# Performance work log

Hardware: AMD Instinct MI355X
Metric: run time of the kernel (lower is better)

The kernel has to match this reference:

```python
import jax, jax.numpy as jnp
import numpy as np

B, I, O, G, D = 2048, 128, 128, 8, 2  # batch, input_dim, output_dim, num_grids, num_dim (complex algebra)
RHO = 1.0
EPS = 1e-5  # BatchNorm1d default eps
GRID_MIN, GRID_MAX = -2.0, 2.0


def _make_cayley():
    # Complex-number geometric algebra: metric=[-1], basis {1, e1}, e1*e1 = -1.
    # (a*b)_z = sum_{x,y} a_x b_y C[x,y,z]
    C = np.zeros((2, 2, 2), dtype=np.float32)
    C[0, 0, 0] = 1.0
    C[0, 1, 1] = 1.0
    C[1, 0, 1] = 1.0
    C[1, 1, 0] = -1.0
    return jnp.asarray(C)


def _make_grid():
    # create_grid2d_full: real varies along axis 0, imag along axis 1 -> (G, G, 2)
    g = jnp.linspace(GRID_MIN, GRID_MAX, G)
    gr, gi = jnp.meshgrid(g, g, indexing='ij')
    return jnp.stack((gr, gi), axis=-1)


def setup_inputs() -> dict:
    key = jax.random.key(0)
    k1, k2 = jax.random.split(key)
    x = jax.random.normal(k1, (B, I, D), dtype=jnp.float32)
    weights = jax.random.normal(k2, (I, O, G, G, D), dtype=jnp.float32)
    silu_weight = jnp.ones((I, O, D), dtype=jnp.float32)
    silu_bias = jnp.zeros((I, O, D), dtype=jnp.float32)
    gamma = jnp.ones((D,), dtype=jnp.float32)   # BatchNorm weight (componentwise)
    beta = jnp.zeros((D,), dtype=jnp.float32)   # BatchNorm bias
    return {
        'x': x,
        'weights': weights,
        'silu_weight': silu_weight,
        'silu_bias': silu_bias,
        'gamma': gamma,
        'beta': beta,
        'grid': _make_grid(),
        'cayley': _make_cayley(),
    }


def reference(x, weights, silu_weight, silu_bias, gamma, beta, grid, cayley):
    # RBF expansion: exp(-||x - grid_point||^2 / rho), complex-algebra norm^2 = a^2 + b^2
    diff = x[:, :, None, None, :] - grid[None, None, :, :, :]        # (B, I, G, G, D)
    rbf = jnp.exp(-jnp.sum(diff * diff, axis=-1) / RHO)              # (B, I, G, G)
    # grid-weight contraction
    res = jnp.einsum('biuv,iouvx->biox', rbf, weights)               # (B, I, O, D)
    # componentwise SiLU branch with Cayley-table (complex) multiplication
    s = jax.nn.silu(x)                                               # (B, I, D)
    sv = jnp.einsum('iox,biy,xyz->bioz', silu_weight, s, cayley)     # (B, I, O, D)
    sv = sv + silu_bias
    out = jnp.sum(res + sv, axis=1)                                  # (B, O, D) -- 'biox->box'
    # componentwise BatchNorm (training mode): stats over (B, O) per component
    mean = jnp.mean(out, axis=(0, 1))
    var = jnp.var(out, axis=(0, 1))
    out = gamma * (out - mean) * jax.lax.rsqrt(var + EPS) + beta
    return out
```

## Files before the change

kernel.cpp:

```cpp
#include <hip/hip_runtime.h>
#include <stdint.h>

typedef unsigned short u16;
typedef __attribute__((ext_vector_type(8))) short bf16x8;
typedef __attribute__((ext_vector_type(4))) float f32x4;

#define B_      2048
#define I_      128
#define O_      128
#define K_MAIN  8192
#define K_TOT   8448
#define N_      256
#define BO      262144
#define NSLICE  16
#define KSTEPS  132

#define W_OFF      0u
#define W_BYTES    (256u*8448u*2u)
#define OUTPS_OFF  (W_OFF + W_BYTES)
#define OUTPS_BYTES (16u*524288u*4u)
#define OUTRED_OFF (OUTPS_OFF + OUTPS_BYTES)
#define OUTRED_BYTES (524288u*4u)
#define BSUM_OFF   (OUTRED_OFF + OUTRED_BYTES)
#define STATS_OFF  (BSUM_OFF + 1024u)

__device__ __forceinline__ float bf2f(u16 u) {
    union { unsigned int i; float f; } c; c.i = ((unsigned int)u) << 16; return c.f;
}
__device__ __forceinline__ u16 f2bf(float f) {
    unsigned int u = __float_as_uint(f);
    return (u16)((u + 0x7fffu + ((u >> 16) & 1u)) >> 16);
}
__device__ __forceinline__ unsigned int pkbf(float lo, float hi) {
    unsigned int ul = __float_as_uint(lo), uh = __float_as_uint(hi);
    ul += 0x7fffu + ((ul >> 16) & 1u);
    uh += 0x7fffu + ((uh >> 16) & 1u);
    return __builtin_amdgcn_perm(uh, ul, 0x07060302);
}
__device__ __forceinline__ float loadF(const void* p, long idx, bool isbf) {
    return isbf ? bf2f(((const u16*)p)[idx]) : ((const float*)p)[idx];
}

#define GLD16(gsrc, ldst) __builtin_amdgcn_global_load_lds( \
    (const __attribute__((address_space(1))) void*)(gsrc),  \
    (__attribute__((address_space(3))) void*)(ldst), 16, 0, 0)

__global__ __launch_bounds__(256) void pack_w(const void* wgt, const void* sw,
                                              const void* sb, u16* W, float* bsum,
                                              float* stats, const u16* flag) {
    bool isbf = (flag[0] == 0x3F80u);
    if (blockIdx.x < 1024) {
        int gid = blockIdx.x * 256 + threadIdx.x;
        int t8 = gid & 15;
        int io = gid >> 4;
        int i = io >> 7, o = io & 127;
        int base = t8 * 8;
        int u = base >> 4, v0 = (base & 15) >> 1;
        long off = ((long)i * 128 + o) * 128 + base;
        float f[8];
        if (isbf) {
            uint4 raw = *(const uint4*)((const u16*)wgt + off);
            const u16* h = (const u16*)&raw;
#pragma unroll
            for (int j = 0; j < 8; ++j) f[j] = bf2f(h[j]);
        } else {
            float4 a = *(const float4*)((const float*)wgt + off);
            float4 bq = *(const float4*)((const float*)wgt + off + 4);
            f[0]=a.x; f[1]=a.y; f[2]=a.z; f[3]=a.w;
            f[4]=bq.x; f[5]=bq.y; f[6]=bq.z; f[7]=bq.w;
        }
        u16 re[4], im[4];
#pragma unroll
        for (int j = 0; j < 4; ++j) { re[j] = f2bf(f[2*j]); im[j] = f2bf(f[2*j+1]); }
        int k = i * 64 + u * 8 + v0;
        *(uint2*)&W[(size_t)(2*o)     * K_TOT + k] = *(const uint2*)re;
        *(uint2*)&W[(size_t)(2*o + 1) * K_TOT + k] = *(const uint2*)im;
    } else if (blockIdx.x < 1280) {
        int e = (blockIdx.x - 1024) * 256 + threadIdx.x;
        int n = e >> 8, j = e & 255;
        int o = n >> 1, xc = n & 1;
        int i = j >> 1, c = j & 1;
        float swr = loadF(sw, (long)(i * 128 + o) * 2, isbf);
        float swi = loadF(sw, (long)(i * 128 + o) * 2 + 1, isbf);
        float v = (xc == 0) ? (c == 0 ? swr : -swi) : (c == 0 ? swi : swr);
        W[(size_t)n * K_TOT + K_MAIN + j] = f2bf(v);
    } else {
        int n = threadIdx.x;
        float s = 0.0f;
#pragma unroll 8
        for (int i = 0; i < 128; ++i) s += loadF(sb, (long)i * 256 + n, isbf);
        bsum[n] = s;
        if (threadIdx.x < 4) stats[threadIdx.x] = 0.0f;
    }
}

#define BM 64
#define BN 256
#define BK 64

__global__ __launch_bounds__(256, 2) void gemm_fused(const void* __restrict__ x,
                                                     const void* __restrict__ grd,
                                                     const u16* __restrict__ W,
                                                     float* __restrict__ out_ps,
                                                     const u16* flag) {
    bool isbf = (flag[0] == 0x3F80u);
    __shared__ u16 As[BM * BK];
    __shared__ u16 Bs[BN * BK];
    int tid = threadIdx.x, lane = tid & 63, w = tid >> 6;
    int wm = w >> 1, wn = w & 1;
    int m0 = blockIdx.y * BM;
    int s = blockIdx.z;
    int quad = lane >> 4, l16 = lane & 15;
    int arow = tid >> 2, q4 = tid & 3;
    int asw = arow & 7;
    int kbeg = (KSTEPS * s) / NSLICE, kend = (KSTEPS * (s + 1)) / NSLICE;

    float g[8];
#pragma unroll
    for (int j = 0; j < 8; ++j) g[j] = loadF(grd, (long)j * 16, isbf);

    f32x4 zero = {0.f, 0.f, 0.f, 0.f};
    f32x4 acc[2][8];
#pragma unroll
    for (int mt = 0; mt < 2; ++mt)
#pragma unroll
        for (int nt = 0; nt < 8; ++nt) acc[mt][nt] = zero;

    for (int kt = kbeg; kt < kend; ++kt) {
        int k0 = kt * 64;
#pragma unroll
        for (int jj = 0; jj < 8; ++jj) {
            int p = (w * 8 + jj) * 64 + lane;
            int r = p >> 3, cph = p & 7;
            int c = cph ^ (r & 7);
            GLD16(W + (size_t)r * K_TOT + k0 + c * 8,
                  Bs + (size_t)p * 8);
        }
        unsigned int op[8];
        if (kt < 128) {
            long xb = ((long)(m0 + arow) * 128 + kt) * 2;
            float vr = loadF(x, xb, isbf);
            float vi = loadF(x, xb + 1, isbf);
            float ei[8];
#pragma unroll
            for (int v = 0; v < 8; ++v) { float d = vi - g[v]; ei[v] = __expf(-d * d); }
#pragma unroll
            for (int uu = 0; uu < 2; ++uu) {
                float d = vr - g[2 * q4 + uu];
                float er = __expf(-d * d);
#pragma unroll
                for (int v = 0; v < 8; v += 2)
                    op[uu * 4 + (v >> 1)] = pkbf(er * ei[v], er * ei[v + 1]);
            }
        } else {
            int t = kt - 128;
            long base = (long)(m0 + arow) * 256 + 64 * t + 16 * q4;
#pragma unroll
            for (int e = 0; e < 16; e += 2) {
                float v0 = loadF(x, base + e, isbf);
                float v1 = loadF(x, base + e + 1, isbf);
                float s0 = v0 / (1.0f + __expf(-v0));
                float s1 = v1 / (1.0f + __expf(-v1));
                op[e >> 1] = pkbf(s0, s1);
            }
        }
        {
            u16* rowbase = As + arow * 64;
            *(uint4*)(rowbase + (((2 * q4)     ^ asw) << 3)) = ((const uint4*)op)[0];
            *(uint4*)(rowbase + (((2 * q4 + 1) ^ asw) << 3)) = ((const uint4*)op)[1];
        }
        __syncthreads();
#pragma unroll
        for (int ks = 0; ks < 2; ++ks) {
            bf16x8 fa[2], fb[8];
#pragma unroll
            for (int mt = 0; mt < 2; ++mt) {
                int r = wm * 32 + mt * 16 + l16;
                fa[mt] = *(const bf16x8*)&As[r * 64 + (((ks * 4 + quad) ^ (r & 7)) << 3)];
            }
#pragma unroll
            for (int nt = 0; nt < 8; ++nt) {
                int r = wn * 128 + nt * 16 + l16;
                fb[nt] = *(const bf16x8*)&Bs[r * 64 + (((ks * 4 + quad) ^ (r & 7)) << 3)];
            }
#pragma unroll
            for (int mt = 0; mt < 2; ++mt)
#pragma unroll
                for (int nt = 0; nt < 8; ++nt)
                    acc[mt][nt] = __builtin_amdgcn_mfma_f32_16x16x32_bf16(
                        fa[mt], fb[nt], acc[mt][nt], 0, 0, 0);
        }
        __syncthreads();
    }
    float* outp = out_ps + (size_t)s * 524288;
    int mbase = m0 + wm * 32 + quad * 4;
    int nbase = wn * 128 + l16;
#pragma unroll
    for (int mt = 0; mt < 2; ++mt)
#pragma unroll
        for (int nt = 0; nt < 8; ++nt) {
            int n = nbase + nt * 16;
#pragma unroll
            for (int r = 0; r < 4; ++r) {
                int m = mbase + mt * 16 + r;
                outp[(size_t)m * N_ + n] = acc[mt][nt][r];
            }
        }
}

__global__ void stats_red(const float* __restrict__ out_ps, const float* __restrict__ bsum,
                          float* __restrict__ out_red, float* stats) {
    int gid = blockIdx.x * 256 + threadIdx.x;
    int o = gid & 127;
    float vr = 0.f, vi = 0.f;
#pragma unroll
    for (int s = 0; s < NSLICE; ++s) {
        float2 p = *(const float2*)(out_ps + (size_t)s * 524288 + (size_t)gid * 2);
        vr += p.x; vi += p.y;
    }
    vr += bsum[o * 2]; vi += bsum[o * 2 + 1];
    float2 ov; ov.x = vr; ov.y = vi;
    *(float2*)(out_red + (size_t)gid * 2) = ov;
    float sr = vr, si = vi, qr = vr * vr, qi = vi * vi;
    for (int off = 32; off > 0; off >>= 1) {
        sr += __shfl_down(sr, off);
        si += __shfl_down(si, off);
        qr += __shfl_down(qr, off);
        qi += __shfl_down(qi, off);
    }
    __shared__ float red[4][4];
    int lane = threadIdx.x & 63, w = threadIdx.x >> 6;
    if (lane == 0) { red[w][0] = sr; red[w][1] = si; red[w][2] = qr; red[w][3] = qi; }
    __syncthreads();
    if (threadIdx.x < 4) {
        float t = red[0][threadIdx.x] + red[1][threadIdx.x] +
                  red[2][threadIdx.x] + red[3][threadIdx.x];
        atomicAdd(&stats[threadIdx.x], t);
    }
}

__global__ void norm_k(const float* __restrict__ out_red, const float* __restrict__ stats,
                       const void* gamma, const void* beta, void* out, const u16* flag) {
    bool isbf = (flag[0] == 0x3F80u);
    int gid = blockIdx.x * 256 + threadIdx.x;
    const float inv = 1.0f / (float)BO;
    float mr = stats[0] * inv, mi = stats[1] * inv;
    float varr = stats[2] * inv - mr * mr;
    float vari = stats[3] * inv - mi * mi;
    float gr = loadF(gamma, 0, isbf), gi = loadF(gamma, 1, isbf);
    float br = loadF(beta, 0, isbf),  bi = loadF(beta, 1, isbf);
    float scr = gr * rsqrtf(varr + 1e-5f);
    float sci = gi * rsqrtf(vari + 1e-5f);
    float2 v = *(const float2*)(out_red + (size_t)gid * 2);
    float rr = (v.x - mr) * scr + br;
    float ri = (v.y - mi) * sci + bi;
    if (isbf) {
        unsigned int packed = pkbf(rr, ri);
        *(unsigned int*)((u16*)out + (size_t)gid * 2) = packed;
    } else {
        ((float*)out)[(size_t)gid * 2]     = rr;
        ((float*)out)[(size_t)gid * 2 + 1] = ri;
    }
}

extern "C" void kernel_launch(void* const* d_in, const int* in_sizes, int n_in,
                              void* d_out, int out_size, void* d_ws, size_t ws_size,
                              hipStream_t stream) {
    const void* x     = d_in[0];
    const void* wgt   = d_in[1];
    const void* sw    = d_in[2];
    const void* sb    = d_in[3];
    const void* gamma = d_in[4];
    const void* beta  = d_in[5];
    const void* grd   = d_in[6];
    const u16* flag = (const u16*)gamma;

    uint8_t* ws = (uint8_t*)d_ws;
    u16*   W       = (u16*)(ws + W_OFF);
    float* out_ps  = (float*)(ws + OUTPS_OFF);
    float* out_red = (float*)(ws + OUTRED_OFF);
    float* bsum    = (float*)(ws + BSUM_OFF);
    float* stats   = (float*)(ws + STATS_OFF);

    pack_w<<<1281, 256, 0, stream>>>(wgt, sw, sb, W, bsum, stats, flag);
    gemm_fused<<<dim3(1, B_ / BM, NSLICE), 256, 0, stream>>>(x, grd, W, out_ps, flag);
    stats_red<<<1024, 256, 0, stream>>>(out_ps, bsum, out_red, stats);
    norm_k<<<1024, 256, 0, stream>>>(out_red, stats, gamma, beta, d_out, flag);
}
```

Measured before the change: 132.3 us.

## Reduce split-K partial sums with global atomics instead of a partial buffer

The GEMM slices no longer write per-slice partial outputs to a 16x workspace that a separate pass then sums. Each slice now atomically adds its results straight into a single zero-initialised output buffer, which the weight-pack kernel clears. The stats kernel only reads the reduced values, and the bias sum is applied in both stats and normalisation. This removes the large partial write and reread, but adds 16-way float atomic contention per element and makes the summation order nondeterministic.

```diff
diff --git a/kernel.cpp b/kernel.cpp
--- a/kernel.cpp
+++ b/kernel.cpp
@@ -17,9 +17,7 @@
 
 #define W_OFF      0u
 #define W_BYTES    (256u*8448u*2u)
-#define OUTPS_OFF  (W_OFF + W_BYTES)
-#define OUTPS_BYTES (16u*524288u*4u)
-#define OUTRED_OFF (OUTPS_OFF + OUTPS_BYTES)
+#define OUTRED_OFF (W_OFF + W_BYTES)
 #define OUTRED_BYTES (524288u*4u)
 #define BSUM_OFF   (OUTRED_OFF + OUTRED_BYTES)
 #define STATS_OFF  (BSUM_OFF + 1024u)
@@ -47,7 +45,8 @@
 
 __global__ __launch_bounds__(256) void pack_w(const void* wgt, const void* sw,
                                               const void* sb, u16* W, float* bsum,
-                                              float* stats, const u16* flag) {
+                                              float* stats, float* out_red,
+                                              const u16* flag) {
     bool isbf = (flag[0] == 0x3F80u);
     if (blockIdx.x < 1024) {
         int gid = blockIdx.x * 256 + threadIdx.x;
@@ -84,13 +83,17 @@
         float swi = loadF(sw, (long)(i * 128 + o) * 2 + 1, isbf);
         float v = (xc == 0) ? (c == 0 ? swr : -swi) : (c == 0 ? swi : swr);
         W[(size_t)n * K_TOT + K_MAIN + j] = f2bf(v);
-    } else {
+    } else if (blockIdx.x == 1280) {
         int n = threadIdx.x;
         float s = 0.0f;
 #pragma unroll 8
         for (int i = 0; i < 128; ++i) s += loadF(sb, (long)i * 256 + n, isbf);
         bsum[n] = s;
         if (threadIdx.x < 4) stats[threadIdx.x] = 0.0f;
+    } else {
+        int g2 = (blockIdx.x - 1281) * 256 + threadIdx.x;
+        float2 z; z.x = 0.f; z.y = 0.f;
+        *(float2*)(out_red + (size_t)g2 * 2) = z;
     }
 }
 
@@ -101,7 +104,7 @@
 __global__ __launch_bounds__(256, 2) void gemm_fused(const void* __restrict__ x,
                                                      const void* __restrict__ grd,
                                                      const u16* __restrict__ W,
-                                                     float* __restrict__ out_ps,
+                                                     float* __restrict__ out_red,
                                                      const u16* flag) {
     bool isbf = (flag[0] == 0x3F80u);
     __shared__ u16 As[BM * BK];
@@ -192,7 +195,6 @@
         }
         __syncthreads();
     }
-    float* outp = out_ps + (size_t)s * 524288;
     int mbase = m0 + wm * 32 + quad * 4;
     int nbase = wn * 128 + l16;
 #pragma unroll
@@ -203,24 +205,18 @@
 #pragma unroll
             for (int r = 0; r < 4; ++r) {
                 int m = mbase + mt * 16 + r;
-                outp[(size_t)m * N_ + n] = acc[mt][nt][r];
-            }
-        }
-}
-
-__global__ void stats_red(const float* __restrict__ out_ps, const float* __restrict__ bsum,
-                          float* __restrict__ out_red, float* stats) {
+                atomicAdd(&out_red[(size_t)m * N_ + n], acc[mt][nt][r]);
+            }
+        }
+}
+
+__global__ void stats_k(const float* __restrict__ out_red, const float* __restrict__ bsum,
+                        float* stats) {
     int gid = blockIdx.x * 256 + threadIdx.x;
     int o = gid & 127;
-    float vr = 0.f, vi = 0.f;
-#pragma unroll
-    for (int s = 0; s < NSLICE; ++s) {
-        float2 p = *(const float2*)(out_ps + (size_t)s * 524288 + (size_t)gid * 2);
-        vr += p.x; vi += p.y;
-    }
-    vr += bsum[o * 2]; vi += bsum[o * 2 + 1];
-    float2 ov; ov.x = vr; ov.y = vi;
-    *(float2*)(out_red + (size_t)gid * 2) = ov;
+    float2 p = *(const float2*)(out_red + (size_t)gid * 2);
+    float vr = p.x + bsum[o * 2];
+    float vi = p.y + bsum[o * 2 + 1];
     float sr = vr, si = vi, qr = vr * vr, qi = vi * vi;
     for (int off = 32; off > 0; off >>= 1) {
         sr += __shfl_down(sr, off);
@@ -239,10 +235,12 @@
     }
 }
 
-__global__ void norm_k(const float* __restrict__ out_red, const float* __restrict__ stats,
-                       const void* gamma, const void* beta, void* out, const u16* flag) {
+__global__ void norm_k(const float* __restrict__ out_red, const float* __restrict__ bsum,
+                       const float* __restrict__ stats, const void* gamma,
+                       const void* beta, void* out, const u16* flag) {
     bool isbf = (flag[0] == 0x3F80u);
     int gid = blockIdx.x * 256 + threadIdx.x;
+    int o = gid & 127;
     const float inv = 1.0f / (float)BO;
     float mr = stats[0] * inv, mi = stats[1] * inv;
     float varr = stats[2] * inv - mr * mr;
@@ -252,8 +250,8 @@
     float scr = gr * rsqrtf(varr + 1e-5f);
     float sci = gi * rsqrtf(vari + 1e-5f);
     float2 v = *(const float2*)(out_red + (size_t)gid * 2);
-    float rr = (v.x - mr) * scr + br;
-    float ri = (v.y - mi) * sci + bi;
+    float rr = (v.x + bsum[o * 2]     - mr) * scr + br;
+    float ri = (v.y + bsum[o * 2 + 1] - mi) * sci + bi;
     if (isbf) {
         unsigned int packed = pkbf(rr, ri);
         *(unsigned int*)((u16*)out + (size_t)gid * 2) = packed;
@@ -277,13 +275,12 @@
 
     uint8_t* ws = (uint8_t*)d_ws;
     u16*   W       = (u16*)(ws + W_OFF);
-    float* out_ps  = (float*)(ws + OUTPS_OFF);
     float* out_red = (float*)(ws + OUTRED_OFF);
     float* bsum    = (float*)(ws + BSUM_OFF);
     float* stats   = (float*)(ws + STATS_OFF);
 
-    pack_w<<<1281, 256, 0, stream>>>(wgt, sw, sb, W, bsum, stats, flag);
-    gemm_fused<<<dim3(1, B_ / BM, NSLICE), 256, 0, stream>>>(x, grd, W, out_ps, flag);
-    stats_red<<<1024, 256, 0, stream>>>(out_ps, bsum, out_red, stats);
-    norm_k<<<1024, 256, 0, stream>>>(out_red, stats, gamma, beta, d_out, flag);
-}
+    pack_w<<<2305, 256, 0, stream>>>(wgt, sw, sb, W, bsum, stats, out_red, flag);
+    gemm_fused<<<dim3(1, B_ / BM, NSLICE), 256, 0, stream>>>(x, grd, W, out_red, flag);
+    stats_k<<<1024, 256, 0, stream>>>(out_red, bsum, stats);
+    norm_k<<<1024, 256, 0, stream>>>(out_red, bsum, stats, gamma, beta, d_out, flag);
+}
```

After: 148.1 us. 1.12x slower.

## Double-buffer LDS tiles to overlap W loads and RBF compute with MFMA

Applied to the files above, without the earlier changes.

Doubles the shared-memory buffers for the A and B tiles in the fused GEMM. The next W tile is issued right after a single barrier per k-step. The next A tile (RBF/SiLU values) is computed into the alternate buffer after the MFMA loop. The aim is to hide global-load latency and drop one barrier per iteration. In exchange, LDS use doubles to about 80 KB per block, which may limit occupancy at two blocks per CU.

```diff
diff --git a/kernel.cpp b/kernel.cpp
--- a/kernel.cpp
+++ b/kernel.cpp
@@ -98,14 +98,45 @@
 #define BN 256
 #define BK 64
 
+__device__ __forceinline__ void computeA(const void* x, const float* g, int m0, int arow,
+                                         int q4, int kt, bool isbf, unsigned int* op) {
+    if (kt < 128) {
+        long xb = ((long)(m0 + arow) * 128 + kt) * 2;
+        float vr = loadF(x, xb, isbf);
+        float vi = loadF(x, xb + 1, isbf);
+        float ei[8];
+#pragma unroll
+        for (int v = 0; v < 8; ++v) { float d = vi - g[v]; ei[v] = __expf(-d * d); }
+#pragma unroll
+        for (int uu = 0; uu < 2; ++uu) {
+            float d = vr - g[2 * q4 + uu];
+            float er = __expf(-d * d);
+#pragma unroll
+            for (int v = 0; v < 8; v += 2)
+                op[uu * 4 + (v >> 1)] = pkbf(er * ei[v], er * ei[v + 1]);
+        }
+    } else {
+        int t = kt - 128;
+        long base = (long)(m0 + arow) * 256 + 64 * t + 16 * q4;
+#pragma unroll
+        for (int e = 0; e < 16; e += 2) {
+            float v0 = loadF(x, base + e, isbf);
+            float v1 = loadF(x, base + e + 1, isbf);
+            float s0 = v0 / (1.0f + __expf(-v0));
+            float s1 = v1 / (1.0f + __expf(-v1));
+            op[e >> 1] = pkbf(s0, s1);
+        }
+    }
+}
+
 __global__ __launch_bounds__(256, 2) void gemm_fused(const void* __restrict__ x,
                                                      const void* __restrict__ grd,
                                                      const u16* __restrict__ W,
                                                      float* __restrict__ out_ps,
                                                      const u16* flag) {
     bool isbf = (flag[0] == 0x3F80u);
-    __shared__ u16 As[BM * BK];
-    __shared__ u16 Bs[BN * BK];
+    __shared__ u16 As[2 * BM * BK];
+    __shared__ u16 Bs[2 * BN * BK];
     int tid = threadIdx.x, lane = tid & 63, w = tid >> 6;
     int wm = w >> 1, wn = w & 1;
     int m0 = blockIdx.y * BM;
@@ -126,62 +157,47 @@
 #pragma unroll
         for (int nt = 0; nt < 8; ++nt) acc[mt][nt] = zero;
 
+#define ISSUE_B(KT, BUF) do { int k0 = (KT) * 64;                          \
+    _Pragma("unroll")                                                      \
+    for (int jj = 0; jj < 8; ++jj) {                                       \
+        int p = (w * 8 + jj) * 64 + lane;                                  \
+        int r = p >> 3, cph = p & 7;                                       \
+        int c = cph ^ (r & 7);                                             \
+        GLD16(W + (size_t)r * K_TOT + k0 + c * 8,                          \
+              Bs + (size_t)(BUF) * (BN * BK) + (size_t)p * 8);             \
+    } } while (0)
+
+#define WRITE_A(BUF, OP) do {                                              \
+    u16* rowbase = As + (BUF) * (BM * BK) + arow * 64;                     \
+    *(uint4*)(rowbase + (((2 * q4)     ^ asw) << 3)) = ((const uint4*)(OP))[0]; \
+    *(uint4*)(rowbase + (((2 * q4 + 1) ^ asw) << 3)) = ((const uint4*)(OP))[1]; \
+    } while (0)
+
+    {
+        ISSUE_B(kbeg, 0);
+        unsigned int op[8];
+        computeA(x, g, m0, arow, q4, kbeg, isbf, op);
+        WRITE_A(0, op);
+    }
+
     for (int kt = kbeg; kt < kend; ++kt) {
-        int k0 = kt * 64;
-#pragma unroll
-        for (int jj = 0; jj < 8; ++jj) {
-            int p = (w * 8 + jj) * 64 + lane;
-            int r = p >> 3, cph = p & 7;
-            int c = cph ^ (r & 7);
-            GLD16(W + (size_t)r * K_TOT + k0 + c * 8,
-                  Bs + (size_t)p * 8);
-        }
-        unsigned int op[8];
-        if (kt < 128) {
-            long xb = ((long)(m0 + arow) * 128 + kt) * 2;
-            float vr = loadF(x, xb, isbf);
-            float vi = loadF(x, xb + 1, isbf);
-            float ei[8];
-#pragma unroll
-            for (int v = 0; v < 8; ++v) { float d = vi - g[v]; ei[v] = __expf(-d * d); }
-#pragma unroll
-            for (int uu = 0; uu < 2; ++uu) {
-                float d = vr - g[2 * q4 + uu];
-                float er = __expf(-d * d);
-#pragma unroll
-                for (int v = 0; v < 8; v += 2)
-                    op[uu * 4 + (v >> 1)] = pkbf(er * ei[v], er * ei[v + 1]);
-            }
-        } else {
-            int t = kt - 128;
-            long base = (long)(m0 + arow) * 256 + 64 * t + 16 * q4;
-#pragma unroll
-            for (int e = 0; e < 16; e += 2) {
-                float v0 = loadF(x, base + e, isbf);
-                float v1 = loadF(x, base + e + 1, isbf);
-                float s0 = v0 / (1.0f + __expf(-v0));
-                float s1 = v1 / (1.0f + __expf(-v1));
-                op[e >> 1] = pkbf(s0, s1);
-            }
-        }
-        {
-            u16* rowbase = As + arow * 64;
-            *(uint4*)(rowbase + (((2 * q4)     ^ asw) << 3)) = ((const uint4*)op)[0];
-            *(uint4*)(rowbase + (((2 * q4 + 1) ^ asw) << 3)) = ((const uint4*)op)[1];
-        }
+        int cur = (kt - kbeg) & 1, nxt = cur ^ 1;
         __syncthreads();
+        if (kt + 1 < kend) ISSUE_B(kt + 1, nxt);
+        const u16* Ac = As + cur * (BM * BK);
+        const u16* Bc = Bs + cur * (BN * BK);
 #pragma unroll
         for (int ks = 0; ks < 2; ++ks) {
             bf16x8 fa[2], fb[8];
 #pragma unroll
             for (int mt = 0; mt < 2; ++mt) {
                 int r = wm * 32 + mt * 16 + l16;
-                fa[mt] = *(const bf16x8*)&As[r * 64 + (((ks * 4 + quad) ^ (r & 7)) << 3)];
+                fa[mt] = *(const bf16x8*)&Ac[r * 64 + (((ks * 4 + quad) ^ (r & 7)) << 3)];
             }
 #pragma unroll
             for (int nt = 0; nt < 8; ++nt) {
                 int r = wn * 128 + nt * 16 + l16;
-                fb[nt] = *(const bf16x8*)&Bs[r * 64 + (((ks * 4 + quad) ^ (r & 7)) << 3)];
+                fb[nt] = *(const bf16x8*)&Bc[r * 64 + (((ks * 4 + quad) ^ (r & 7)) << 3)];
             }
 #pragma unroll
             for (int mt = 0; mt < 2; ++mt)
@@ -190,7 +206,11 @@
                     acc[mt][nt] = __builtin_amdgcn_mfma_f32_16x16x32_bf16(
                         fa[mt], fb[nt], acc[mt][nt], 0, 0, 0);
         }
-        __syncthreads();
+        if (kt + 1 < kend) {
+            unsigned int op[8];
+            computeA(x, g, m0, arow, q4, kt + 1, isbf, op);
+            WRITE_A(nxt, op);
+        }
     }
     float* outp = out_ps + (size_t)s * 524288;
     int mbase = m0 + wm * 32 + quad * 4;
```

After: 135.7 us. 1.03x slower.

## Drop LDS staging; load MFMA fragments directly from global into registers

Applied to the files above, without the earlier changes.

Removes the shared-memory tiles and both barriers from the fused GEMM. Each wave now loads its B fragments straight from global memory and builds its own A operand fragments (RBF and SiLU values) in registers. The aim is to cut LDS traffic and synchronisation stalls. In exchange, A-side work is duplicated across waves (each wn pair recomputes the same exps), and B loads become uncoalesced, strided 16-byte reads that depend on L2/L1 reuse.

```diff
diff --git a/kernel.cpp b/kernel.cpp
--- a/kernel.cpp
+++ b/kernel.cpp
@@ -40,10 +40,6 @@
 __device__ __forceinline__ float loadF(const void* p, long idx, bool isbf) {
     return isbf ? bf2f(((const u16*)p)[idx]) : ((const float*)p)[idx];
 }
-
-#define GLD16(gsrc, ldst) __builtin_amdgcn_global_load_lds( \
-    (const __attribute__((address_space(1))) void*)(gsrc),  \
-    (__attribute__((address_space(3))) void*)(ldst), 16, 0, 0)
 
 __global__ __launch_bounds__(256) void pack_w(const void* wgt, const void* sw,
                                               const void* sb, u16* W, float* bsum,
@@ -96,7 +92,6 @@
 
 #define BM 64
 #define BN 256
-#define BK 64
 
 __global__ __launch_bounds__(256, 2) void gemm_fused(const void* __restrict__ x,
                                                      const void* __restrict__ grd,
@@ -104,20 +99,19 @@
                                                      float* __restrict__ out_ps,
                                                      const u16* flag) {
     bool isbf = (flag[0] == 0x3F80u);
-    __shared__ u16 As[BM * BK];
-    __shared__ u16 Bs[BN * BK];
     int tid = threadIdx.x, lane = tid & 63, w = tid >> 6;
     int wm = w >> 1, wn = w & 1;
     int m0 = blockIdx.y * BM;
     int s = blockIdx.z;
     int quad = lane >> 4, l16 = lane & 15;
-    int arow = tid >> 2, q4 = tid & 3;
-    int asw = arow & 7;
     int kbeg = (KSTEPS * s) / NSLICE, kend = (KSTEPS * (s + 1)) / NSLICE;
 
     float g[8];
 #pragma unroll
     for (int j = 0; j < 8; ++j) g[j] = loadF(grd, (long)j * 16, isbf);
+
+    const u16* Wb = W + (size_t)(wn * 128 + l16) * K_TOT;
+    int r0 = m0 + wm * 32 + l16;
 
     f32x4 zero = {0.f, 0.f, 0.f, 0.f};
     f32x4 acc[2][8];
@@ -127,70 +121,61 @@
         for (int nt = 0; nt < 8; ++nt) acc[mt][nt] = zero;
 
     for (int kt = kbeg; kt < kend; ++kt) {
-        int k0 = kt * 64;
-#pragma unroll
-        for (int jj = 0; jj < 8; ++jj) {
-            int p = (w * 8 + jj) * 64 + lane;
-            int r = p >> 3, cph = p & 7;
-            int c = cph ^ (r & 7);
-            GLD16(W + (size_t)r * K_TOT + k0 + c * 8,
-                  Bs + (size_t)p * 8);
-        }
-        unsigned int op[8];
+        bf16x8 fb[8][2];
+#pragma unroll
+        for (int nt = 0; nt < 8; ++nt)
+#pragma unroll
+            for (int ks = 0; ks < 2; ++ks)
+                fb[nt][ks] = *(const bf16x8*)&Wb[(size_t)(nt * 16) * K_TOT
+                                                 + kt * 64 + ks * 32 + quad * 8];
+        bf16x8 fa[2][2];
         if (kt < 128) {
-            long xb = ((long)(m0 + arow) * 128 + kt) * 2;
-            float vr = loadF(x, xb, isbf);
-            float vi = loadF(x, xb + 1, isbf);
-            float ei[8];
-#pragma unroll
-            for (int v = 0; v < 8; ++v) { float d = vi - g[v]; ei[v] = __expf(-d * d); }
-#pragma unroll
-            for (int uu = 0; uu < 2; ++uu) {
-                float d = vr - g[2 * q4 + uu];
-                float er = __expf(-d * d);
-#pragma unroll
-                for (int v = 0; v < 8; v += 2)
-                    op[uu * 4 + (v >> 1)] = pkbf(er * ei[v], er * ei[v + 1]);
+#pragma unroll
+            for (int mt = 0; mt < 2; ++mt) {
+                long xb = ((long)(r0 + mt * 16) * 128 + kt) * 2;
+                float xr = loadF(x, xb, isbf);
+                float xi = loadF(x, xb + 1, isbf);
+                float ei[8];
+#pragma unroll
+                for (int v = 0; v < 8; ++v) { float d = xi - g[v]; ei[v] = __expf(-d * d); }
+#pragma unroll
+                for (int ks = 0; ks < 2; ++ks) {
+                    float d = xr - g[ks * 4 + quad];
+                    float er = __expf(-d * d);
+                    unsigned int op[4];
+#pragma unroll
+                    for (int j = 0; j < 4; ++j)
+                        op[j] = pkbf(er * ei[2 * j], er * ei[2 * j + 1]);
+                    fa[mt][ks] = *(const bf16x8*)op;
+                }
             }
         } else {
             int t = kt - 128;
-            long base = (long)(m0 + arow) * 256 + 64 * t + 16 * q4;
-#pragma unroll
-            for (int e = 0; e < 16; e += 2) {
-                float v0 = loadF(x, base + e, isbf);
-                float v1 = loadF(x, base + e + 1, isbf);
-                float s0 = v0 / (1.0f + __expf(-v0));
-                float s1 = v1 / (1.0f + __expf(-v1));
-                op[e >> 1] = pkbf(s0, s1);
-            }
+#pragma unroll
+            for (int mt = 0; mt < 2; ++mt)
+#pragma unroll
+                for (int ks = 0; ks < 2; ++ks) {
+                    long base = (long)(r0 + mt * 16) * 256 + 64 * t + ks * 32 + quad * 8;
+                    unsigned int op[4];
+#pragma unroll
+                    for (int e = 0; e < 8; e += 2) {
+                        float v0 = loadF(x, base + e, isbf);
+                        float v1 = loadF(x, base + e + 1, isbf);
+                        float s0 = v0 / (1.0f + __expf(-v0));
+                        float s1 = v1 / (1.0f + __expf(-v1));
+                        op[e >> 1] = pkbf(s0, s1);
+                    }
+                    fa[mt][ks] = *(const bf16x8*)op;
+                }
         }
-        {
-            u16* rowbase = As + arow * 64;
-            *(uint4*)(rowbase + (((2 * q4)     ^ asw) << 3)) = ((const uint4*)op)[0];
-            *(uint4*)(rowbase + (((2 * q4 + 1) ^ asw) << 3)) = ((const uint4*)op)[1];
-        }
-        __syncthreads();
-#pragma unroll
-        for (int ks = 0; ks < 2; ++ks) {
-            bf16x8 fa[2], fb[8];
-#pragma unroll
-            for (int mt = 0; mt < 2; ++mt) {
-                int r = wm * 32 + mt * 16 + l16;
-                fa[mt] = *(const bf16x8*)&As[r * 64 + (((ks * 4 + quad) ^ (r & 7)) << 3)];
-            }
-#pragma unroll
-            for (int nt = 0; nt < 8; ++nt) {
-                int r = wn * 128 + nt * 16 + l16;
-                fb[nt] = *(const bf16x8*)&Bs[r * 64 + (((ks * 4 + quad) ^ (r & 7)) << 3)];
-            }
+#pragma unroll
+        for (int ks = 0; ks < 2; ++ks)
 #pragma unroll
             for (int mt = 0; mt < 2; ++mt)
 #pragma unroll
                 for (int nt = 0; nt < 8; ++nt)
                     acc[mt][nt] = __builtin_amdgcn_mfma_f32_16x16x32_bf16(
-                        fa[mt], fb[nt], acc[mt][nt], 0, 0, 0);
-        }
-        __syncthreads();
+                        fa[mt][ks], fb[nt][ks], acc[mt][nt], 0, 0, 0);
     }
     float* outp = out_ps + (size_t)s * 524288;
     int mbase = m0 + wm * 32 + quad * 4;
```

Result: slower. 164.8 us (+24.6%).
